# Optimization experiments

Measured on AMD Instinct MI355X. Metric: run time of the kernel, lower is better.

Reference implementation:

```python
import jax, jax.numpy as jnp
import numpy as np

LEAKY_SLOPE = 0.2  # DGL GATConv default negative_slope


def setup_inputs() -> dict:
    key = jax.random.key(0)
    ks = jax.random.split(key, 10)
    N_SRC, N_DST, E = 100000, 100000, 1600000
    H1, H0, D = 2, 2, 32          # in_h1_heads, in_h0_heads (GAT num_heads), out_dim
    IN1, IN0 = 128, 128           # in_h1_dim, in_h0_dim
    OUT_HEADS = 4
    return {
        "hier_1": jax.random.normal(ks[0], (N_SRC, H1, IN1), jnp.float32),
        "hier_0": jax.random.normal(ks[1], (N_DST, IN0), jnp.float32),
        "src_idx": jax.random.randint(ks[2], (E,), 0, N_SRC, jnp.int32),
        "dst_idx": jax.random.randint(ks[3], (E,), 0, N_DST, jnp.int32),
        "W_src": jax.random.normal(ks[4], (H0 * D, IN1), jnp.float32) * 0.05,
        "W_dst": jax.random.normal(ks[5], (H0 * D, IN0), jnp.float32) * 0.05,
        "attn_l": jax.random.normal(ks[6], (H0, D), jnp.float32) * 0.1,
        "attn_r": jax.random.normal(ks[7], (H0, D), jnp.float32) * 0.1,
        "gat_bias": jnp.zeros((H0, D), jnp.float32),
        "fc_W": jax.random.normal(ks[8], (OUT_HEADS, H1 * H0), jnp.float32),
        "fc_b": jnp.zeros((OUT_HEADS,), jnp.float32),
    }


def reference(hier_1, hier_0, src_idx, dst_idx, W_src, W_dst,
              attn_l, attn_r, gat_bias, fc_W, fc_b):
    N_src, H1, _ = hier_1.shape
    N_dst = hier_0.shape[0]
    H0, D = attn_l.shape

    # Shared GATConv projections (same weights reused across the H1 python loop
    # in the original -> vectorize over the H1 axis).
    feat_src = jnp.einsum('nhi,oi->nho', hier_1, W_src).reshape(N_src, H1, H0, D)
    feat_dst = (hier_0 @ W_dst.T).reshape(N_dst, H0, D)

    el = jnp.einsum('nhkd,kd->nhk', feat_src, attn_l)   # [N_src, H1, H0]
    er = jnp.einsum('nkd,kd->nk', feat_dst, attn_r)     # [N_dst, H0]

    # Edge attention logits + softmax over incoming edges per dst node.
    e = jax.nn.leaky_relu(el[src_idx] + er[dst_idx][:, None, :], LEAKY_SLOPE)  # [E,H1,H0]
    emax = jax.ops.segment_max(e, dst_idx, num_segments=N_dst)
    emax = jnp.where(jnp.isfinite(emax), emax, 0.0)     # zero-in-degree safety
    ee = jnp.exp(e - emax[dst_idx])
    denom = jax.ops.segment_sum(ee, dst_idx, num_segments=N_dst)
    alpha = ee / denom[dst_idx]                          # [E, H1, H0]

    # Aggregate messages: sum_e alpha * feat_src[src].
    msg = alpha[..., None] * feat_src[src_idx]           # [E, H1, H0, D]
    out = jax.ops.segment_sum(msg, dst_idx, num_segments=N_dst)  # [N_dst,H1,H0,D]
    out = out + gat_bias[None, None]                     # GATConv bias (per call)

    # cat over H1 (H1-major), transpose, softmax-normalized linear head mixing.
    res = out.reshape(N_dst, H1 * H0, D)
    res = jnp.swapaxes(res, 1, 2)                        # [N_dst, D, H1*H0]
    W = jax.nn.softmax(fc_W, axis=1)                     # normWeight: softmax(dim=1)
    res = res @ W.T + fc_b                               # [N_dst, D, out_heads]
    return jnp.swapaxes(res, 1, 2)                       # [N_dst, out_heads, D]
```

## Files before the change

kernel.cpp:

```cpp
#include <hip/hip_runtime.h>
#include <hip/hip_bf16.h>

typedef __attribute__((ext_vector_type(8))) short short8_t;
typedef __attribute__((ext_vector_type(4))) float float4v;

__device__ __forceinline__ float lrelu(float x) { return x > 0.f ? x : 0.2f * x; }
__device__ __forceinline__ float blo(unsigned u) { return __uint_as_float(u << 16); }
__device__ __forceinline__ float bhi(unsigned u) { return __uint_as_float(u & 0xffff0000u); }

__device__ __forceinline__ short8_t mk8(unsigned a, unsigned b, unsigned c, unsigned d) {
    union { unsigned u[4]; short8_t s; } x;
    x.u[0] = a; x.u[1] = b; x.u[2] = c; x.u[3] = d;
    return x.s;
}

__global__ void k_prep(const float* __restrict__ Wdst,
                       const float* __restrict__ attn_r,
                       const float* __restrict__ fcW,
                       const float* __restrict__ fcb,
                       const float* __restrict__ Wsrc,
                       float* __restrict__ w_er, float* __restrict__ Wn,
                       float* __restrict__ fb,
                       unsigned short* __restrict__ Wb_hi,
                       unsigned short* __restrict__ Wb_lo) {
    int t = threadIdx.x;
#pragma unroll
    for (int j = 0; j < 32; ++j) {
        int i = t + j * 256;
        float x = Wsrc[i];
        unsigned hb = __float_as_uint(x) & 0xffff0000u;
        float lf = x - __uint_as_float(hb);
        Wb_hi[i] = (unsigned short)(hb >> 16);
        Wb_lo[i] = (unsigned short)(__float_as_uint(lf) >> 16);
    }
    {
        int h0 = t >> 7, i = t & 127;
        float s = 0.f;
        for (int d = 0; d < 32; ++d)
            s += attn_r[h0 * 32 + d] * Wdst[(size_t)(h0 * 32 + d) * 128 + i];
        w_er[t] = s;
    }
    if (t < 16) {
        int oh = t >> 2, k = t & 3;
        float w[4], m = -1e30f;
        for (int j = 0; j < 4; ++j) {
            w[j] = fcW[oh * 4 + j];
            m = fmaxf(m, w[j]);
        }
        float s = 0.f;
        for (int j = 0; j < 4; ++j) s += __expf(w[j] - m);
        Wn[t] = __expf(w[k] - m) / s;
    }
    if (t < 4) fb[t] = fcb[t];
}

__global__ __launch_bounds__(256) void k_featA(
        const float* __restrict__ hier1,
        const unsigned short* __restrict__ Wb_hi,
        const unsigned short* __restrict__ Wb_lo,
        const float* __restrict__ attn_l,
        const float* __restrict__ hier0, const float* __restrict__ w_er,
        const int* __restrict__ dstIdx,
        __hip_bfloat16* __restrict__ featb, float* __restrict__ el,
        float* __restrict__ er, int* __restrict__ deg,
        int nrows, int Ndst, int E, int ntiles) {
    int t = threadIdx.x;
    int w = t >> 6, lane = t & 63;

    for (int e = blockIdx.x * 256 + t; e < E; e += gridDim.x * 256)
        atomicAdd(&deg[dstIdx[e]], 1);

    int lr = lane & 15;
    int lg = lane >> 4;

    for (int tile = blockIdx.x * 4 + w; tile < ntiles; tile += gridDim.x * 4) {
        int m0 = tile * 16;

        short8_t a_hi[4], a_lo[4];
        int row_l = m0 + lr;
        if (row_l >= nrows) row_l = nrows - 1;
        const float* hrow = hier1 + (size_t)row_l * 128 + lg * 8;
#pragma unroll
        for (int kc = 0; kc < 4; ++kc) {
            float4 f0 = *reinterpret_cast<const float4*>(hrow + kc * 32);
            float4 f1 = *reinterpret_cast<const float4*>(hrow + kc * 32 + 4);
            float xs[8] = {f0.x, f0.y, f0.z, f0.w, f1.x, f1.y, f1.z, f1.w};
            unsigned h[4], l4[4];
#pragma unroll
            for (int p = 0; p < 4; ++p) {
                unsigned b0 = __float_as_uint(xs[2 * p]);
                unsigned b1 = __float_as_uint(xs[2 * p + 1]);
                unsigned h0b = b0 & 0xffff0000u, h1b = b1 & 0xffff0000u;
                h[p] = (h0b >> 16) | h1b;
                float l0 = xs[2 * p] - __uint_as_float(h0b);
                float l1 = xs[2 * p + 1] - __uint_as_float(h1b);
                l4[p] = (__float_as_uint(l0) >> 16) | (__float_as_uint(l1) & 0xffff0000u);
            }
            a_hi[kc] = mk8(h[0], h[1], h[2], h[3]);
            a_lo[kc] = mk8(l4[0], l4[1], l4[2], l4[3]);
        }

        float4v acc[4];
#pragma unroll
        for (int n = 0; n < 4; ++n) acc[n] = (float4v){0.f, 0.f, 0.f, 0.f};
#pragma unroll
        for (int n = 0; n < 4; ++n) {
            const unsigned short* bh = Wb_hi + (size_t)(n * 16 + lr) * 128 + lg * 8;
            const unsigned short* bl = Wb_lo + (size_t)(n * 16 + lr) * 128 + lg * 8;
#pragma unroll
            for (int kc = 0; kc < 4; ++kc) {
                short8_t Bh = *reinterpret_cast<const short8_t*>(bh + kc * 32);
                short8_t Bl = *reinterpret_cast<const short8_t*>(bl + kc * 32);
                acc[n] = __builtin_amdgcn_mfma_f32_16x16x32_bf16(a_lo[kc], Bh, acc[n], 0, 0, 0);
                acc[n] = __builtin_amdgcn_mfma_f32_16x16x32_bf16(a_hi[kc], Bl, acc[n], 0, 0, 0);
                acc[n] = __builtin_amdgcn_mfma_f32_16x16x32_bf16(a_hi[kc], Bh, acc[n], 0, 0, 0);
            }
        }

        float pe0[4] = {0.f, 0.f, 0.f, 0.f};
        float pe1[4] = {0.f, 0.f, 0.f, 0.f};
#pragma unroll
        for (int n = 0; n < 4; ++n) {
            float al = attn_l[n * 16 + lr];
#pragma unroll
            for (int r = 0; r < 4; ++r) {
                int row = m0 + lg * 4 + r;
                float v = acc[n][r];
                if (row < nrows)
                    featb[((size_t)(row >> 1)) * 128 + (row & 1) * 64 + n * 16 + lr] =
                        __float2bfloat16(v);
                if (n < 2) pe0[r] += v * al; else pe1[r] += v * al;
            }
        }
#pragma unroll
        for (int m = 1; m <= 8; m <<= 1) {
#pragma unroll
            for (int r = 0; r < 4; ++r) {
                pe0[r] += __shfl_xor(pe0[r], m, 64);
                pe1[r] += __shfl_xor(pe1[r], m, 64);
            }
        }
        if (lr < 2) {
#pragma unroll
            for (int r = 0; r < 4; ++r) {
                int row = m0 + lg * 4 + r;
                float ev = lr ? pe1[r] : pe0[r];
                if (row < nrows) el[row * 2 + lr] = ev;
            }
        }
    }

    int gw = blockIdx.x * 4 + w;
    int nwaves = gridDim.x * 4;
    float2 w0 = *reinterpret_cast<const float2*>(w_er + lane * 2);
    float2 w1 = *reinterpret_cast<const float2*>(w_er + 128 + lane * 2);
    for (int node = gw; node < Ndst; node += nwaves) {
        float2 h = *reinterpret_cast<const float2*>(hier0 + (size_t)node * 128 + lane * 2);
        float p0 = h.x * w0.x + h.y * w0.y;
        float p1 = h.x * w1.x + h.y * w1.y;
#pragma unroll
        for (int m = 32; m >= 1; m >>= 1) {
            p0 += __shfl_xor(p0, m, 64);
            p1 += __shfl_xor(p1, m, 64);
        }
        if (lane == 0) {
            er[node * 2] = p0;
            er[node * 2 + 1] = p1;
        }
    }
}

__global__ void k_alloc(const int* __restrict__ deg, int* __restrict__ off,
                        int* __restrict__ cursor, int* __restrict__ counter,
                        int N) {
    int d = blockIdx.x * blockDim.x + threadIdx.x;
    int lane = threadIdx.x & 63;
    int v = (d < N) ? deg[d] : 0;
    int inc = v;
#pragma unroll
    for (int m = 1; m < 64; m <<= 1) {
        int u = __shfl_up(inc, m, 64);
        if (lane >= m) inc += u;
    }
    int excl = inc - v;
    int base = 0;
    if (lane == 63) base = atomicAdd(counter, inc);
    base = __shfl(base, 63, 64);
    if (d < N) {
        off[d] = base + excl;
        cursor[d] = base + excl;
    }
}

__global__ void k_scatter(const int* __restrict__ src, const int* __restrict__ dst,
                          int* __restrict__ cursor, int* __restrict__ ssrc, int E) {
    int e = blockIdx.x * blockDim.x + threadIdx.x;
    if (e >= E) return;
    int pos = atomicAdd(&cursor[dst[e]], 1);
    ssrc[pos] = src[e];
}

__global__ __launch_bounds__(256) void k_gather(
        const int* __restrict__ ssrc, const int* __restrict__ off,
        const int* __restrict__ deg,
        const float* __restrict__ el, const float* __restrict__ er,
        const uint4* __restrict__ feat4,
        const float* __restrict__ bias,
        const float* __restrict__ Wn, const float* __restrict__ fb,
        float* __restrict__ out, int Ndst, int E) {
    __shared__ float g[4][128];
    int t = threadIdx.x;
    int wv = t >> 6, lane = t & 63;
    int d = blockIdx.x * 4 + wv;
    bool valid = d < Ndst;

    int q = lane >> 4;
    int c = lane & 15;
    int k = c >> 2;
    float erk = valid ? er[d * 2 + (k & 1)] : 0.f;
    int start = valid ? off[d] : 0;
    int n = valid ? deg[d] : 0;

    float a[8];
#pragma unroll
    for (int j = 0; j < 8; ++j) a[j] = 0.f;
    float den = 0.f;

    int ai = start + q;
    int s_pre = ssrc[ai < E ? ai : 0];
    for (int i = 0; i < n; i += 4) {
        int s = s_pre;
        int ni = start + i + 4 + q;
        s_pre = ssrc[ni < E ? ni : 0];
        bool ve = (i + q) < n;
        uint4 f = feat4[(size_t)s * 16 + c];
        float eL = el[s * 4 + k];
        float ee = ve ? __expf(lrelu(eL + erk)) : 0.f;
        den += ee;
        a[0] = fmaf(ee, blo(f.x), a[0]);
        a[1] = fmaf(ee, bhi(f.x), a[1]);
        a[2] = fmaf(ee, blo(f.y), a[2]);
        a[3] = fmaf(ee, bhi(f.y), a[3]);
        a[4] = fmaf(ee, blo(f.z), a[4]);
        a[5] = fmaf(ee, bhi(f.z), a[5]);
        a[6] = fmaf(ee, blo(f.w), a[6]);
        a[7] = fmaf(ee, bhi(f.w), a[7]);
    }

#pragma unroll
    for (int m = 16; m <= 32; m <<= 1) {
        den += __shfl_xor(den, m, 64);
#pragma unroll
        for (int j = 0; j < 8; ++j) a[j] += __shfl_xor(a[j], m, 64);
    }

    float inv = den > 0.f ? 1.f / den : 0.f;
    if (q == 0) {
        int h0 = k & 1, ddb = (c & 3) * 8;
#pragma unroll
        for (int j = 0; j < 8; ++j)
            g[wv][c * 8 + j] = a[j] * inv + bias[h0 * 32 + ddb + j];
    }
    __syncthreads();

    if (valid) {
        int dd = (lane & 15) * 2;
        int oh = lane >> 4;
        float r0 = fb[oh], r1 = r0;
#pragma unroll
        for (int kk = 0; kk < 4; ++kk) {
            float wgt = Wn[oh * 4 + kk];
            r0 = fmaf(g[wv][kk * 32 + dd], wgt, r0);
            r1 = fmaf(g[wv][kk * 32 + dd + 1], wgt, r1);
        }
        *reinterpret_cast<float2*>(out + (size_t)d * 128 + lane * 2) =
            make_float2(r0, r1);
    }
}

extern "C" void kernel_launch(void* const* d_in, const int* in_sizes, int n_in,
                              void* d_out, int out_size, void* d_ws, size_t ws_size,
                              hipStream_t stream) {
    (void)n_in; (void)out_size; (void)ws_size;
    const float* hier1  = (const float*)d_in[0];
    const float* hier0  = (const float*)d_in[1];
    const int*   srcIdx = (const int*)d_in[2];
    const int*   dstIdx = (const int*)d_in[3];
    const float* Wsrc   = (const float*)d_in[4];
    const float* Wdst   = (const float*)d_in[5];
    const float* attn_l = (const float*)d_in[6];
    const float* attn_r = (const float*)d_in[7];
    const float* bias   = (const float*)d_in[8];
    const float* fcW    = (const float*)d_in[9];
    const float* fcb    = (const float*)d_in[10];
    float* out = (float*)d_out;

    const int Nsrc  = in_sizes[0] / 256;
    const int Ndst  = in_sizes[1] / 128;
    const int E     = in_sizes[2];
    const int nrows = Nsrc * 2;
    const int ntiles = (nrows + 15) / 16;

    __hip_bfloat16* featb = (__hip_bfloat16*)d_ws;
    unsigned short* Wb_hi = (unsigned short*)(featb + (size_t)Nsrc * 128);
    unsigned short* Wb_lo = Wb_hi + 8192;
    float* el   = (float*)(Wb_lo + 8192);
    float* er   = el   + (size_t)nrows * 2;
    float* w_er = er   + (size_t)Ndst * 2;
    float* Wn   = w_er + 256;
    float* fb   = Wn + 16;
    int*  deg     = (int*)(fb + 4);
    int*  off     = deg + Ndst;
    int*  cursor  = off + Ndst;
    int*  counter = cursor + Ndst;
    int*  ssrc    = counter + 1;

    hipMemsetAsync(deg, 0, (size_t)Ndst * sizeof(int), stream);
    hipMemsetAsync(counter, 0, sizeof(int), stream);

    k_prep<<<1, 256, 0, stream>>>(Wdst, attn_r, fcW, fcb, Wsrc,
                                  w_er, Wn, fb, Wb_hi, Wb_lo);

    int blocksA = (ntiles + 3) / 4;
    if (blocksA < 1) blocksA = 1;
    k_featA<<<blocksA, 256, 0, stream>>>(hier1, Wb_hi, Wb_lo, attn_l,
                                         hier0, w_er, dstIdx,
                                         featb, el, er, deg,
                                         nrows, Ndst, E, ntiles);

    k_alloc<<<(Ndst + 255) / 256, 256, 0, stream>>>(deg, off, cursor, counter, Ndst);

    k_scatter<<<(E + 255) / 256, 256, 0, stream>>>(srcIdx, dstIdx, cursor, ssrc, E);

    k_gather<<<(Ndst + 3) / 4, 256, 0, stream>>>(ssrc, off, deg, el, er,
                                                 (const uint4*)featb,
                                                 bias, Wn, fb, out, Ndst, E);
}
```

Before: 523.6 us.

## Restructure pipeline: separate histogram, fuse scatter into projection, MFMA er kernel

Moves the degree histogram into its own kernel ahead of the prefix-sum allocation. The edge scatter is fused into the feature-projection kernel, with the hier_1 loads issued before the scatter loop so their latency overlaps the atomics. The er projection becomes a separate MFMA-based kernel using split-bf16. The gather loop gains a two-deep prefetch of features and logits. This reorders the whole schedule and adds an extra launch, trading the old grid-stride er loop for a one-tile-per-wave layout.

```diff
diff --git a/kernel.cpp b/kernel.cpp
--- a/kernel.cpp
+++ b/kernel.cpp
@@ -12,6 +12,24 @@
     union { unsigned u[4]; short8_t s; } x;
     x.u[0] = a; x.u[1] = b; x.u[2] = c; x.u[3] = d;
     return x.s;
+}
+
+__device__ __forceinline__ void split8(const float4& f0, const float4& f1,
+                                       short8_t& hi8, short8_t& lo8) {
+    float xs[8] = {f0.x, f0.y, f0.z, f0.w, f1.x, f1.y, f1.z, f1.w};
+    unsigned h[4], l4[4];
+#pragma unroll
+    for (int p = 0; p < 4; ++p) {
+        unsigned b0 = __float_as_uint(xs[2 * p]);
+        unsigned b1 = __float_as_uint(xs[2 * p + 1]);
+        unsigned h0b = b0 & 0xffff0000u, h1b = b1 & 0xffff0000u;
+        h[p] = (h0b >> 16) | h1b;
+        float l0 = xs[2 * p] - __uint_as_float(h0b);
+        float l1 = xs[2 * p + 1] - __uint_as_float(h1b);
+        l4[p] = (__float_as_uint(l0) >> 16) | (__float_as_uint(l1) & 0xffff0000u);
+    }
+    hi8 = mk8(h[0], h[1], h[2], h[3]);
+    lo8 = mk8(l4[0], l4[1], l4[2], l4[3]);
 }
 
 __global__ void k_prep(const float* __restrict__ Wdst,
@@ -54,120 +72,9 @@
     if (t < 4) fb[t] = fcb[t];
 }
 
-__global__ __launch_bounds__(256) void k_featA(
-        const float* __restrict__ hier1,
-        const unsigned short* __restrict__ Wb_hi,
-        const unsigned short* __restrict__ Wb_lo,
-        const float* __restrict__ attn_l,
-        const float* __restrict__ hier0, const float* __restrict__ w_er,
-        const int* __restrict__ dstIdx,
-        __hip_bfloat16* __restrict__ featb, float* __restrict__ el,
-        float* __restrict__ er, int* __restrict__ deg,
-        int nrows, int Ndst, int E, int ntiles) {
-    int t = threadIdx.x;
-    int w = t >> 6, lane = t & 63;
-
-    for (int e = blockIdx.x * 256 + t; e < E; e += gridDim.x * 256)
-        atomicAdd(&deg[dstIdx[e]], 1);
-
-    int lr = lane & 15;
-    int lg = lane >> 4;
-
-    for (int tile = blockIdx.x * 4 + w; tile < ntiles; tile += gridDim.x * 4) {
-        int m0 = tile * 16;
-
-        short8_t a_hi[4], a_lo[4];
-        int row_l = m0 + lr;
-        if (row_l >= nrows) row_l = nrows - 1;
-        const float* hrow = hier1 + (size_t)row_l * 128 + lg * 8;
-#pragma unroll
-        for (int kc = 0; kc < 4; ++kc) {
-            float4 f0 = *reinterpret_cast<const float4*>(hrow + kc * 32);
-            float4 f1 = *reinterpret_cast<const float4*>(hrow + kc * 32 + 4);
-            float xs[8] = {f0.x, f0.y, f0.z, f0.w, f1.x, f1.y, f1.z, f1.w};
-            unsigned h[4], l4[4];
-#pragma unroll
-            for (int p = 0; p < 4; ++p) {
-                unsigned b0 = __float_as_uint(xs[2 * p]);
-                unsigned b1 = __float_as_uint(xs[2 * p + 1]);
-                unsigned h0b = b0 & 0xffff0000u, h1b = b1 & 0xffff0000u;
-                h[p] = (h0b >> 16) | h1b;
-                float l0 = xs[2 * p] - __uint_as_float(h0b);
-                float l1 = xs[2 * p + 1] - __uint_as_float(h1b);
-                l4[p] = (__float_as_uint(l0) >> 16) | (__float_as_uint(l1) & 0xffff0000u);
-            }
-            a_hi[kc] = mk8(h[0], h[1], h[2], h[3]);
-            a_lo[kc] = mk8(l4[0], l4[1], l4[2], l4[3]);
-        }
-
-        float4v acc[4];
-#pragma unroll
-        for (int n = 0; n < 4; ++n) acc[n] = (float4v){0.f, 0.f, 0.f, 0.f};
-#pragma unroll
-        for (int n = 0; n < 4; ++n) {
-            const unsigned short* bh = Wb_hi + (size_t)(n * 16 + lr) * 128 + lg * 8;
-            const unsigned short* bl = Wb_lo + (size_t)(n * 16 + lr) * 128 + lg * 8;
-#pragma unroll
-            for (int kc = 0; kc < 4; ++kc) {
-                short8_t Bh = *reinterpret_cast<const short8_t*>(bh + kc * 32);
-                short8_t Bl = *reinterpret_cast<const short8_t*>(bl + kc * 32);
-                acc[n] = __builtin_amdgcn_mfma_f32_16x16x32_bf16(a_lo[kc], Bh, acc[n], 0, 0, 0);
-                acc[n] = __builtin_amdgcn_mfma_f32_16x16x32_bf16(a_hi[kc], Bl, acc[n], 0, 0, 0);
-                acc[n] = __builtin_amdgcn_mfma_f32_16x16x32_bf16(a_hi[kc], Bh, acc[n], 0, 0, 0);
-            }
-        }
-
-        float pe0[4] = {0.f, 0.f, 0.f, 0.f};
-        float pe1[4] = {0.f, 0.f, 0.f, 0.f};
-#pragma unroll
-        for (int n = 0; n < 4; ++n) {
-            float al = attn_l[n * 16 + lr];
-#pragma unroll
-            for (int r = 0; r < 4; ++r) {
-                int row = m0 + lg * 4 + r;
-                float v = acc[n][r];
-                if (row < nrows)
-                    featb[((size_t)(row >> 1)) * 128 + (row & 1) * 64 + n * 16 + lr] =
-                        __float2bfloat16(v);
-                if (n < 2) pe0[r] += v * al; else pe1[r] += v * al;
-            }
-        }
-#pragma unroll
-        for (int m = 1; m <= 8; m <<= 1) {
-#pragma unroll
-            for (int r = 0; r < 4; ++r) {
-                pe0[r] += __shfl_xor(pe0[r], m, 64);
-                pe1[r] += __shfl_xor(pe1[r], m, 64);
-            }
-        }
-        if (lr < 2) {
-#pragma unroll
-            for (int r = 0; r < 4; ++r) {
-                int row = m0 + lg * 4 + r;
-                float ev = lr ? pe1[r] : pe0[r];
-                if (row < nrows) el[row * 2 + lr] = ev;
-            }
-        }
-    }
-
-    int gw = blockIdx.x * 4 + w;
-    int nwaves = gridDim.x * 4;
-    float2 w0 = *reinterpret_cast<const float2*>(w_er + lane * 2);
-    float2 w1 = *reinterpret_cast<const float2*>(w_er + 128 + lane * 2);
-    for (int node = gw; node < Ndst; node += nwaves) {
-        float2 h = *reinterpret_cast<const float2*>(hier0 + (size_t)node * 128 + lane * 2);
-        float p0 = h.x * w0.x + h.y * w0.y;
-        float p1 = h.x * w1.x + h.y * w1.y;
-#pragma unroll
-        for (int m = 32; m >= 1; m >>= 1) {
-            p0 += __shfl_xor(p0, m, 64);
-            p1 += __shfl_xor(p1, m, 64);
-        }
-        if (lane == 0) {
-            er[node * 2] = p0;
-            er[node * 2 + 1] = p1;
-        }
-    }
+__global__ void k_hist(const int* __restrict__ dst, int* __restrict__ deg, int E) {
+    int e = blockIdx.x * blockDim.x + threadIdx.x;
+    if (e < E) atomicAdd(&deg[dst[e]], 1);
 }
 
 __global__ void k_alloc(const int* __restrict__ deg, int* __restrict__ off,
@@ -192,12 +99,149 @@
     }
 }
 
-__global__ void k_scatter(const int* __restrict__ src, const int* __restrict__ dst,
-                          int* __restrict__ cursor, int* __restrict__ ssrc, int E) {
-    int e = blockIdx.x * blockDim.x + threadIdx.x;
-    if (e >= E) return;
-    int pos = atomicAdd(&cursor[dst[e]], 1);
-    ssrc[pos] = src[e];
+__global__ __launch_bounds__(256) void k_featA(
+        const float* __restrict__ hier1,
+        const unsigned short* __restrict__ Wb_hi,
+        const unsigned short* __restrict__ Wb_lo,
+        const float* __restrict__ attn_l,
+        const int* __restrict__ srcIdx, const int* __restrict__ dstIdx,
+        int* __restrict__ cursor, int* __restrict__ ssrc,
+        __hip_bfloat16* __restrict__ featb, float* __restrict__ el,
+        int nrows, int E, int ntiles) {
+    int t = threadIdx.x;
+    int w = t >> 6, lane = t & 63;
+    int lr = lane & 15;
+    int lg = lane >> 4;
+
+    int tile = blockIdx.x * 4 + w;
+    bool hasTile = tile < ntiles;
+    int m0 = tile * 16;
+
+    float4 areg[8];
+    if (hasTile) {
+        int row_l = m0 + lr;
+        if (row_l >= nrows) row_l = nrows - 1;
+        const float* hrow = hier1 + (size_t)row_l * 128 + lg * 8;
+#pragma unroll
+        for (int kc = 0; kc < 4; ++kc) {
+            areg[2 * kc]     = *reinterpret_cast<const float4*>(hrow + kc * 32);
+            areg[2 * kc + 1] = *reinterpret_cast<const float4*>(hrow + kc * 32 + 4);
+        }
+    }
+
+    for (int e = blockIdx.x * 256 + t; e < E; e += gridDim.x * 256) {
+        int s = srcIdx[e];
+        int d = dstIdx[e];
+        int pos = atomicAdd(&cursor[d], 1);
+        ssrc[pos] = s;
+    }
+
+    if (!hasTile) return;
+
+    short8_t a_hi[4], a_lo[4];
+#pragma unroll
+    for (int kc = 0; kc < 4; ++kc)
+        split8(areg[2 * kc], areg[2 * kc + 1], a_hi[kc], a_lo[kc]);
+
+    float4v acc[4];
+#pragma unroll
+    for (int n = 0; n < 4; ++n) acc[n] = (float4v){0.f, 0.f, 0.f, 0.f};
+#pragma unroll
+    for (int n = 0; n < 4; ++n) {
+        const unsigned short* bh = Wb_hi + (size_t)(n * 16 + lr) * 128 + lg * 8;
+        const unsigned short* bl = Wb_lo + (size_t)(n * 16 + lr) * 128 + lg * 8;
+#pragma unroll
+        for (int kc = 0; kc < 4; ++kc) {
+            short8_t Bh = *reinterpret_cast<const short8_t*>(bh + kc * 32);
+            short8_t Bl = *reinterpret_cast<const short8_t*>(bl + kc * 32);
+            acc[n] = __builtin_amdgcn_mfma_f32_16x16x32_bf16(a_lo[kc], Bh, acc[n], 0, 0, 0);
+            acc[n] = __builtin_amdgcn_mfma_f32_16x16x32_bf16(a_hi[kc], Bl, acc[n], 0, 0, 0);
+            acc[n] = __builtin_amdgcn_mfma_f32_16x16x32_bf16(a_hi[kc], Bh, acc[n], 0, 0, 0);
+        }
+    }
+
+    float pe0[4] = {0.f, 0.f, 0.f, 0.f};
+    float pe1[4] = {0.f, 0.f, 0.f, 0.f};
+#pragma unroll
+    for (int n = 0; n < 4; ++n) {
+        float al = attn_l[n * 16 + lr];
+#pragma unroll
+        for (int r = 0; r < 4; ++r) {
+            int row = m0 + lg * 4 + r;
+            float v = acc[n][r];
+            if (row < nrows)
+                featb[((size_t)(row >> 1)) * 128 + (row & 1) * 64 + n * 16 + lr] =
+                    __float2bfloat16(v);
+            if (n < 2) pe0[r] += v * al; else pe1[r] += v * al;
+        }
+    }
+#pragma unroll
+    for (int m = 1; m <= 8; m <<= 1) {
+#pragma unroll
+        for (int r = 0; r < 4; ++r) {
+            pe0[r] += __shfl_xor(pe0[r], m, 64);
+            pe1[r] += __shfl_xor(pe1[r], m, 64);
+        }
+    }
+    if (lr < 2) {
+#pragma unroll
+        for (int r = 0; r < 4; ++r) {
+            int row = m0 + lg * 4 + r;
+            float ev = lr ? pe1[r] : pe0[r];
+            if (row < nrows) el[row * 2 + lr] = ev;
+        }
+    }
+}
+
+__global__ __launch_bounds__(256) void k_er(
+        const float* __restrict__ hier0, const float* __restrict__ w_er,
+        float* __restrict__ er, int Ndst, int ntilesE) {
+    int t = threadIdx.x;
+    int w = t >> 6, lane = t & 63;
+    int lr = lane & 15, lg = lane >> 4;
+
+    int tile = blockIdx.x * 4 + w;
+    if (tile >= ntilesE) return;
+    int m0 = tile * 16;
+
+    short8_t Bh[4], Bl[4];
+#pragma unroll
+    for (int kc = 0; kc < 4; ++kc) {
+        Bh[kc] = mk8(0, 0, 0, 0);
+        Bl[kc] = mk8(0, 0, 0, 0);
+    }
+    if (lr < 2) {
+#pragma unroll
+        for (int kc = 0; kc < 4; ++kc) {
+            float4 f0 = *reinterpret_cast<const float4*>(w_er + lr * 128 + kc * 32 + lg * 8);
+            float4 f1 = *reinterpret_cast<const float4*>(w_er + lr * 128 + kc * 32 + lg * 8 + 4);
+            split8(f0, f1, Bh[kc], Bl[kc]);
+        }
+    }
+
+    int node = m0 + lr;
+    if (node >= Ndst) node = Ndst - 1;
+    const float* hrow = hier0 + (size_t)node * 128 + lg * 8;
+
+    float4v acc = (float4v){0.f, 0.f, 0.f, 0.f};
+#pragma unroll
+    for (int kc = 0; kc < 4; ++kc) {
+        float4 f0 = *reinterpret_cast<const float4*>(hrow + kc * 32);
+        float4 f1 = *reinterpret_cast<const float4*>(hrow + kc * 32 + 4);
+        short8_t a_hi, a_lo;
+        split8(f0, f1, a_hi, a_lo);
+        acc = __builtin_amdgcn_mfma_f32_16x16x32_bf16(a_lo, Bh[kc], acc, 0, 0, 0);
+        acc = __builtin_amdgcn_mfma_f32_16x16x32_bf16(a_hi, Bl[kc], acc, 0, 0, 0);
+        acc = __builtin_amdgcn_mfma_f32_16x16x32_bf16(a_hi, Bh[kc], acc, 0, 0, 0);
+    }
+
+    if (lr < 2) {
+#pragma unroll
+        for (int r = 0; r < 4; ++r) {
+            int nn = m0 + lg * 4 + r;
+            if (nn < Ndst) er[nn * 2 + lr] = acc[r];
+        }
+    }
 }
 
 __global__ __launch_bounds__(256) void k_gather(
@@ -226,25 +270,31 @@
     for (int j = 0; j < 8; ++j) a[j] = 0.f;
     float den = 0.f;
 
-    int ai = start + q;
-    int s_pre = ssrc[ai < E ? ai : 0];
+    int base = start + q;
+    int sA = ssrc[base < E ? base : 0];
+    int sB = ssrc[(base + 4) < E ? (base + 4) : 0];
+    uint4 fA = feat4[(size_t)sA * 16 + c];
+    float eA = el[sA * 4 + k];
+
     for (int i = 0; i < n; i += 4) {
-        int s = s_pre;
-        int ni = start + i + 4 + q;
-        s_pre = ssrc[ni < E ? ni : 0];
+        uint4 fB = feat4[(size_t)sB * 16 + c];
+        float eB = el[sB * 4 + k];
+        int nx = base + i + 8;
+        int sC = ssrc[nx < E ? nx : 0];
+
         bool ve = (i + q) < n;
-        uint4 f = feat4[(size_t)s * 16 + c];
-        float eL = el[s * 4 + k];
-        float ee = ve ? __expf(lrelu(eL + erk)) : 0.f;
+        float ee = ve ? __expf(lrelu(eA + erk)) : 0.f;
         den += ee;
-        a[0] = fmaf(ee, blo(f.x), a[0]);
-        a[1] = fmaf(ee, bhi(f.x), a[1]);
-        a[2] = fmaf(ee, blo(f.y), a[2]);
-        a[3] = fmaf(ee, bhi(f.y), a[3]);
-        a[4] = fmaf(ee, blo(f.z), a[4]);
-        a[5] = fmaf(ee, bhi(f.z), a[5]);
-        a[6] = fmaf(ee, blo(f.w), a[6]);
-        a[7] = fmaf(ee, bhi(f.w), a[7]);
+        a[0] = fmaf(ee, blo(fA.x), a[0]);
+        a[1] = fmaf(ee, bhi(fA.x), a[1]);
+        a[2] = fmaf(ee, blo(fA.y), a[2]);
+        a[3] = fmaf(ee, bhi(fA.y), a[3]);
+        a[4] = fmaf(ee, blo(fA.z), a[4]);
+        a[5] = fmaf(ee, bhi(fA.z), a[5]);
+        a[6] = fmaf(ee, blo(fA.w), a[6]);
+        a[7] = fmaf(ee, bhi(fA.w), a[7]);
+
+        sB = sC; fA = fB; eA = eB;
     }
 
 #pragma unroll
@@ -299,7 +349,8 @@
     const int Ndst  = in_sizes[1] / 128;
     const int E     = in_sizes[2];
     const int nrows = Nsrc * 2;
-    const int ntiles = (nrows + 15) / 16;
+    const int ntiles  = (nrows + 15) / 16;
+    const int ntilesE = (Ndst + 15) / 16;
 
     __hip_bfloat16* featb = (__hip_bfloat16*)d_ws;
     unsigned short* Wb_hi = (unsigned short*)(featb + (size_t)Nsrc * 128);
@@ -321,16 +372,17 @@
     k_prep<<<1, 256, 0, stream>>>(Wdst, attn_r, fcW, fcb, Wsrc,
                                   w_er, Wn, fb, Wb_hi, Wb_lo);
 
+    k_hist<<<(E + 255) / 256, 256, 0, stream>>>(dstIdx, deg, E);
+
+    k_alloc<<<(Ndst + 255) / 256, 256, 0, stream>>>(deg, off, cursor, counter, Ndst);
+
     int blocksA = (ntiles + 3) / 4;
     if (blocksA < 1) blocksA = 1;
     k_featA<<<blocksA, 256, 0, stream>>>(hier1, Wb_hi, Wb_lo, attn_l,
-                                         hier0, w_er, dstIdx,
-                                         featb, el, er, deg,
-                                         nrows, Ndst, E, ntiles);
-
-    k_alloc<<<(Ndst + 255) / 256, 256, 0, stream>>>(deg, off, cursor, counter, Ndst);
-
-    k_scatter<<<(E + 255) / 256, 256, 0, stream>>>(srcIdx, dstIdx, cursor, ssrc, E);
+                                         srcIdx, dstIdx, cursor, ssrc,
+                                         featb, el, nrows, E, ntiles);
+
+    k_er<<<(ntilesE + 3) / 4, 256, 0, stream>>>(hier0, w_er, er, Ndst, ntilesE);
 
     k_gather<<<(Ndst + 3) / 4, 256, 0, stream>>>(ssrc, off, deg, el, er,
                                                  (const uint4*)featb,
```

Result: faster. 486.8 us (-7.0%).
